# Kernel tuning notes

Measured on AMD Instinct MI355X. Metric: run time of the kernel, lower is better.

## Reference

```python
import jax, jax.numpy as jnp
import numpy as np

EMB = 768
HEADS = 12
HD = EMB // HEADS
FF = 4 * EMB
EPS = 1e-5


def gelu_tanh(x):
    c = jnp.sqrt(jnp.asarray(2.0 / jnp.pi, x.dtype))
    return 0.5 * x * (1.0 + jnp.tanh(c * (x + 0.044715 * x ** 3)))


def layernorm(x, scale, shift):
    mean = x.mean(-1, keepdims=True)
    var = ((x - mean) ** 2).mean(-1, keepdims=True)
    return scale * (x - mean) / jnp.sqrt(var + EPS) + shift


def setup_inputs() -> dict:
    key = jax.random.key(0)
    ks = jax.random.split(key, 12)
    s = 0.02
    return {
        "x": jax.random.normal(ks[0], (8, 1024, EMB), jnp.float32),
        "Wq": jax.random.normal(ks[1], (EMB, EMB), jnp.float32) * s,
        "Wk": jax.random.normal(ks[2], (EMB, EMB), jnp.float32) * s,
        "Wv": jax.random.normal(ks[3], (EMB, EMB), jnp.float32) * s,
        "Wo": jax.random.normal(ks[4], (EMB, EMB), jnp.float32) * s,
        "bo": jnp.zeros((EMB,), jnp.float32),
        "W1": jax.random.normal(ks[5], (EMB, FF), jnp.float32) * s,
        "b1": jnp.zeros((FF,), jnp.float32),
        "W2": jax.random.normal(ks[6], (FF, EMB), jnp.float32) * s,
        "b2": jnp.zeros((EMB,), jnp.float32),
        "ln1_scale": jnp.ones((EMB,), jnp.float32),
        "ln1_shift": jnp.zeros((EMB,), jnp.float32),
        "ln2_scale": jnp.ones((EMB,), jnp.float32),
        "ln2_shift": jnp.zeros((EMB,), jnp.float32),
    }


def reference(x, Wq, Wk, Wv, Wo, bo, W1, b1, W2, b2,
              ln1_scale, ln1_shift, ln2_scale, ln2_shift):
    B, T, _ = x.shape
    inp = x
    h = layernorm(x, ln1_scale, ln1_shift)
    # QKV projections (no bias, qkv_bias=False)
    q = (h @ Wq).reshape(B, T, HEADS, HD).transpose(0, 2, 1, 3)  # [B,H,T,hd]
    k = (h @ Wk).reshape(B, T, HEADS, HD).transpose(0, 2, 1, 3)
    v = (h @ Wv).reshape(B, T, HEADS, HD).transpose(0, 2, 1, 3)
    scores = jnp.einsum('bhqd,bhkd->bhqk', q, k)
    causal = jnp.triu(jnp.ones((T, T), bool), k=1)
    scores = jnp.where(causal, -jnp.inf, scores)
    attn = jax.nn.softmax(scores / jnp.sqrt(jnp.asarray(HD, x.dtype)), axis=-1)
    ctx = jnp.einsum('bhqk,bhkd->bhqd', attn, v)
    ctx = ctx.transpose(0, 2, 1, 3).reshape(B, T, EMB)
    attn_out = ctx @ Wo + bo
    x = inp + attn_out  # dropout is identity (rate 0 / eval)
    inp = x
    h = layernorm(x, ln2_scale, ln2_shift)
    ff = gelu_tanh(h @ W1 + b1) @ W2 + b2
    return inp + ff
```

## Files before the change

kernel.cpp:

```cpp
#include <hip/hip_runtime.h>
#include <hip/hip_bf16.h>
#include <stdint.h>
#include <stddef.h>

#define EMB 768
#define FFD 3072
#define NHEAD 12
#define HD 64
#define SEQ 1024
#define NTOK 8192
#define QKVW 2304

typedef unsigned short u16;
typedef __attribute__((ext_vector_type(8))) short short8;
typedef __attribute__((ext_vector_type(4))) float f32x4;

__device__ __forceinline__ u16 f2bf(float f) {
  union { float f; uint32_t u; } w; w.f = f;
  uint32_t x = w.u + 0x7fffu + ((w.u >> 16) & 1u);
  return (u16)(x >> 16);
}

__device__ __forceinline__ uint32_t pkbf(float lo, float hi) {
  __hip_bfloat162 h = __float22bfloat162_rn(float2{lo, hi});
  union { __hip_bfloat162 h; uint32_t u; } cv; cv.h = h;
  return cv.u;
}

__device__ __forceinline__ void g2l16(const void* g, void* l) {
  __builtin_amdgcn_global_load_lds(
      (const __attribute__((address_space(1))) void*)g,
      (__attribute__((address_space(3))) void*)l, 16, 0, 0);
}

__global__ __launch_bounds__(256)
void transpose_kernel(const float* __restrict__ in, u16* __restrict__ out, int K, int N) {
  __shared__ float tile[32][33];
  const int n0 = blockIdx.x * 32, k0 = blockIdx.y * 32;
  const int tx = threadIdx.x & 31;
  const int ty = threadIdx.x >> 5;
#pragma unroll
  for (int i = 0; i < 32; i += 8)
    tile[ty + i][tx] = in[(size_t)(k0 + ty + i) * N + n0 + tx];
  __syncthreads();
#pragma unroll
  for (int i = 0; i < 32; i += 8)
    out[(size_t)(n0 + ty + i) * K + k0 + tx] = f2bf(tile[tx][ty + i]);
}

__global__ __launch_bounds__(256)
void transpose_qkv_kernel(const float* __restrict__ Wq, const float* __restrict__ Wk,
                          const float* __restrict__ Wv, u16* __restrict__ out) {
  __shared__ float tile[32][33];
  const float* in = blockIdx.z == 0 ? Wq : (blockIdx.z == 1 ? Wk : Wv);
  u16* o = out + (size_t)blockIdx.z * EMB * EMB;
  const int n0 = blockIdx.x * 32, k0 = blockIdx.y * 32;
  const int tx = threadIdx.x & 31;
  const int ty = threadIdx.x >> 5;
#pragma unroll
  for (int i = 0; i < 32; i += 8)
    tile[ty + i][tx] = in[(size_t)(k0 + ty + i) * EMB + n0 + tx];
  __syncthreads();
#pragma unroll
  for (int i = 0; i < 32; i += 8)
    o[(size_t)(n0 + ty + i) * EMB + k0 + tx] = f2bf(tile[tx][ty + i]);
}

__global__ __launch_bounds__(256)
void ln_kernel(const float* __restrict__ x, const float* __restrict__ sc,
               const float* __restrict__ sh, u16* __restrict__ out) {
  const int row = blockIdx.x;
  const int tid = threadIdx.x;
  const float* xr = x + (size_t)row * EMB;
  float v0 = xr[tid], v1 = xr[tid + 256], v2 = xr[tid + 512];
  float s = v0 + v1 + v2;
  float ss = v0 * v0 + v1 * v1 + v2 * v2;
#pragma unroll
  for (int m = 1; m < 64; m <<= 1) { s += __shfl_xor(s, m, 64); ss += __shfl_xor(ss, m, 64); }
  __shared__ float red[8];
  const int wave = tid >> 6, lane = tid & 63;
  if (lane == 0) { red[wave] = s; red[wave + 4] = ss; }
  __syncthreads();
  s = red[0] + red[1] + red[2] + red[3];
  ss = red[4] + red[5] + red[6] + red[7];
  const float mean = s * (1.f / EMB);
  const float var = ss * (1.f / EMB) - mean * mean;
  const float inv = rsqrtf(var + 1e-5f);
  u16* orow = out + (size_t)row * EMB;
  orow[tid]       = f2bf((v0 - mean) * inv * sc[tid]       + sh[tid]);
  orow[tid + 256] = f2bf((v1 - mean) * inv * sc[tid + 256] + sh[tid + 256]);
  orow[tid + 512] = f2bf((v2 - mean) * inv * sc[tid + 512] + sh[tid + 512]);
}

template <int EPI, int MT>
__global__ __launch_bounds__(256)
void gemm_kernel(const u16* __restrict__ A, const u16* __restrict__ BT,
                 void* __restrict__ Cp, const float* __restrict__ bias,
                 const float* __restrict__ res, u16* __restrict__ vTp,
                 int M, int N, int K) {
  constexpr int MI = MT / 32;
  __shared__ u16 As[MT * 64];
  __shared__ u16 Bs[128 * 64];

  const int nwg = gridDim.x * gridDim.y;
  const int orig = blockIdx.y * gridDim.x + blockIdx.x;
  const int swz = (orig & 7) * (nwg >> 3) + (orig >> 3);
  const int m0 = (swz / gridDim.x) * MT;
  const int n0 = (swz % gridDim.x) * 128;

  const int tid = threadIdx.x;
  const int wave = tid >> 6, lane = tid & 63;
  const int wr = wave >> 1, wc = wave & 1;
  const int r = lane & 15, g = lane >> 4;
  const int lrow = lane >> 3;
  const int lelem = (lane & 7) * 8;

  f32x4 acc[MI][4] = {};

  const int nkt = K >> 6;
  for (int kt = 0; kt < nkt; ++kt) {
    const int k0 = kt << 6;
    if (kt) __syncthreads();
#pragma unroll
    for (int q = 0; q < MT / 32; ++q) {
      const int chunk = q * 4 + wave;
      const int row = chunk * 8 + lrow;
      const int e = lelem ^ ((row & 7) << 3);
      g2l16(A + (size_t)(m0 + row) * K + k0 + e, As + chunk * 512);
    }
#pragma unroll
    for (int q = 0; q < 4; ++q) {
      const int chunk = q * 4 + wave;
      const int row = chunk * 8 + lrow;
      const int e = lelem ^ ((row & 7) << 3);
      g2l16(BT + (size_t)(n0 + row) * K + k0 + e, Bs + chunk * 512);
    }
    __syncthreads();
#pragma unroll
    for (int kk = 0; kk < 2; ++kk) {
      short8 af[MI], bf[4];
#pragma unroll
      for (int mi = 0; mi < MI; ++mi) {
        const int row = wr * (MT / 2) + mi * 16 + r;
        af[mi] = *(const short8*)(As + row * 64 + ((kk * 32 + g * 8) ^ ((row & 7) << 3)));
      }
#pragma unroll
      for (int ni = 0; ni < 4; ++ni) {
        const int row = wc * 64 + ni * 16 + r;
        bf[ni] = *(const short8*)(Bs + row * 64 + ((kk * 32 + g * 8) ^ ((row & 7) << 3)));
      }
#pragma unroll
      for (int mi = 0; mi < MI; ++mi)
#pragma unroll
        for (int ni = 0; ni < 4; ++ni)
          acc[mi][ni] = __builtin_amdgcn_mfma_f32_16x16x32_bf16(af[mi], bf[ni], acc[mi][ni], 0, 0, 0);
    }
  }

#pragma unroll
  for (int mi = 0; mi < MI; ++mi)
#pragma unroll
    for (int ni = 0; ni < 4; ++ni) {
      const int rowb = m0 + wr * (MT / 2) + mi * 16 + 4 * g;
      const int col = n0 + wc * 64 + ni * 16 + r;
      if constexpr (EPI == 3) {
        u16 pk[4];
#pragma unroll
        for (int j = 0; j < 4; ++j) pk[j] = f2bf(acc[mi][ni][j]);
        if (col < 1536) {
#pragma unroll
          for (int j = 0; j < 4; ++j)
            ((u16*)Cp)[(size_t)(rowb + j) * N + col] = pk[j];
        } else {
          uint2 w2;
          w2.x = (uint32_t)pk[0] | ((uint32_t)pk[1] << 16);
          w2.y = (uint32_t)pk[2] | ((uint32_t)pk[3] << 16);
          *(uint2*)(vTp + (size_t)(col - 1536) * NTOK + rowb) = w2;
        }
      } else {
#pragma unroll
        for (int j = 0; j < 4; ++j) {
          const size_t idx = (size_t)(rowb + j) * N + col;
          float v = acc[mi][ni][j];
          if constexpr (EPI == 1) {
            ((float*)Cp)[idx] = v + bias[col] + res[idx];
          } else {
            float t = v + bias[col];
            float e = __expf(1.5957691216057308f * (t + 0.044715f * t * t * t));
            float th = 1.f - 2.f / (e + 1.f);
            ((u16*)Cp)[idx] = f2bf(0.5f * t * (1.f + th));
          }
        }
      }
    }
}

#define CEXP 0.18033688011112042f

__global__ __launch_bounds__(256, 3)
void attn_kernel(const u16* __restrict__ qkv, const u16* __restrict__ vT,
                 u16* __restrict__ ctx) {
  const int bh = blockIdx.x;
  const int qt = blockIdx.y;
  const int b = bh / NHEAD, h = bh % NHEAD;
  const int tid = threadIdx.x;
  const int wave = tid >> 6, lane = tid & 63;
  const int r = lane & 15, g = lane >> 4;

  __shared__ u16 Kb[2][64 * 64];
  __shared__ u16 Vb[2][64 * 64];
  __shared__ u16 Pt[4][16 * 64];

  const int qw = qt * 128 + wave * 32;
  const int tok0 = b * SEQ;

  short8 aq[2][2];
#pragma unroll
  for (int qf = 0; qf < 2; ++qf) {
    const u16* qb = qkv + (size_t)(tok0 + qw + qf * 16 + r) * QKVW + h * HD;
    aq[qf][0] = *(const short8*)(qb + g * 8);
    aq[qf][1] = *(const short8*)(qb + 32 + g * 8);
  }

  float l_st[2] = {0.f, 0.f};
  f32x4 oc[2][4] = {};

  const int sr = tid >> 3;
  const int sc = (tid & 7) * 8;
  const int nt = 2 * qt + 2;

  const u16* kg = qkv + (size_t)tok0 * QKVW + EMB + h * HD;
  const u16* vg = vT + (size_t)(h * HD) * NTOK + tok0;
  const int e0 = sc ^ ((sr & 7) << 3);

  auto stage = [&](int buf, int kt) {
    const size_t koff = (size_t)kt * 64;
    u16* kb = (u16*)Kb[buf] + wave * 512;
    u16* vb = (u16*)Vb[buf] + wave * 512;
    g2l16(kg + (koff + sr) * QKVW + e0, kb);
    g2l16(kg + (koff + sr + 32) * QKVW + e0, kb + 2048);
    g2l16(vg + (size_t)sr * NTOK + koff + e0, vb);
    g2l16(vg + (size_t)(sr + 32) * NTOK + koff + e0, vb + 2048);
  };

  stage(0, 0);
  for (int kb = 0; kb < nt; ++kb) {
    __syncthreads();
    const int cur = kb & 1;
    if (kb + 1 < nt) stage(cur ^ 1, kb + 1);

    const int kv0 = kb * 64;
    if (kv0 > qw + 31) continue;

    short8 kf[4][2];
#pragma unroll
    for (int nf = 0; nf < 4; ++nf) {
      const int row = nf * 16 + r;
#pragma unroll
      for (int kk = 0; kk < 2; ++kk)
        kf[nf][kk] = *(const short8*)((char*)Kb[cur] + row * 128 +
                                      ((kk * 64 + g * 16) ^ ((row & 7) << 4)));
    }
    short8 bv[2][4];
#pragma unroll
    for (int half = 0; half < 2; ++half)
#pragma unroll
      for (int nd = 0; nd < 4; ++nd) {
        const int vr = nd * 16 + r;
        bv[half][nd] = *(const short8*)((char*)Vb[cur] + vr * 128 +
                       ((half * 64 + g * 16) ^ ((vr & 7) << 4)));
      }

#pragma unroll
    for (int qf = 0; qf < 2; ++qf) {
      f32x4 st[4];
#pragma unroll
      for (int nf = 0; nf < 4; ++nf) {
        f32x4 z = {};
        z = __builtin_amdgcn_mfma_f32_16x16x32_bf16(kf[nf][0], aq[qf][0], z, 0, 0, 0);
        z = __builtin_amdgcn_mfma_f32_16x16x32_bf16(kf[nf][1], aq[qf][1], z, 0, 0, 0);
        st[nf] = z;
      }
      if (kv0 + 63 > qw + qf * 16) {
        const int qg = qw + qf * 16 + r;
#pragma unroll
        for (int nf = 0; nf < 4; ++nf)
#pragma unroll
          for (int j = 0; j < 4; ++j)
            if (kv0 + nf * 16 + 4 * g + j > qg) st[nf][j] = -3e38f;
      }
      float p[4][4];
      float ps = 0.f;
#pragma unroll
      for (int nf = 0; nf < 4; ++nf)
#pragma unroll
        for (int j = 0; j < 4; ++j) {
          const float pe = exp2f(st[nf][j] * CEXP);
          p[nf][j] = pe;
          ps += pe;
        }
      ps += __shfl_xor(ps, 16);
      ps += __shfl_xor(ps, 32);
      l_st[qf] += ps;

      u16* Pw = (u16*)Pt[wave];
#pragma unroll
      for (int nf = 0; nf < 4; ++nf) {
        uint2 w2;
        w2.x = pkbf(p[nf][0], p[nf][1]);
        w2.y = pkbf(p[nf][2], p[nf][3]);
        *(uint2*)((char*)Pw + r * 128 + ((nf * 32 + g * 8) ^ ((r & 7) << 4))) = w2;
      }
#pragma unroll
      for (int half = 0; half < 2; ++half) {
        short8 pa = *(const short8*)((char*)Pw + r * 128 +
                                     ((half * 64 + g * 16) ^ ((r & 7) << 4)));
#pragma unroll
        for (int nd = 0; nd < 4; ++nd)
          oc[qf][nd] = __builtin_amdgcn_mfma_f32_16x16x32_bf16(pa, bv[half][nd], oc[qf][nd], 0, 0, 0);
      }
    }
  }

#pragma unroll
  for (int qf = 0; qf < 2; ++qf) {
    const float rl = 1.f / l_st[qf];
#pragma unroll
    for (int j = 0; j < 4; ++j) {
      const float rj = __shfl(rl, 4 * g + j, 16);
      const size_t row = (size_t)tok0 + qw + qf * 16 + 4 * g + j;
#pragma unroll
      for (int nd = 0; nd < 4; ++nd)
        ctx[row * EMB + h * HD + nd * 16 + r] = f2bf(oc[qf][nd][j] * rj);
    }
  }
}

extern "C" void kernel_launch(void* const* d_in, const int* in_sizes, int n_in,
                              void* d_out, int out_size, void* d_ws, size_t ws_size,
                              hipStream_t stream) {
  const float* x    = (const float*)d_in[0];
  const float* Wq   = (const float*)d_in[1];
  const float* Wk   = (const float*)d_in[2];
  const float* Wv   = (const float*)d_in[3];
  const float* Wo   = (const float*)d_in[4];
  const float* bo   = (const float*)d_in[5];
  const float* W1   = (const float*)d_in[6];
  const float* b1   = (const float*)d_in[7];
  const float* W2   = (const float*)d_in[8];
  const float* b2   = (const float*)d_in[9];
  const float* ln1s = (const float*)d_in[10];
  const float* ln1b = (const float*)d_in[11];
  const float* ln2s = (const float*)d_in[12];
  const float* ln2b = (const float*)d_in[13];

  char* p = (char*)d_ws;
  u16* qkvT = (u16*)p; p += (size_t)QKVW * EMB * 2;
  u16* woT  = (u16*)p; p += (size_t)EMB * EMB * 2;
  u16* w1T  = (u16*)p; p += (size_t)FFD * EMB * 2;
  u16* w2T  = (u16*)p; p += (size_t)EMB * FFD * 2;
  u16* h1   = (u16*)p; p += (size_t)NTOK * EMB * 2;
  u16* qkv  = (u16*)p; p += (size_t)NTOK * QKVW * 2;
  float* x2 = (float*)p; p += (size_t)NTOK * EMB * 4;
  u16* ff1  = (u16*)p; p += (size_t)NTOK * FFD * 2;
  u16* ctxb = h1;
  u16* h2   = qkv;
  u16* vT   = ff1;

  if (ws_size < (size_t)(p - (char*)d_ws)) return;

  dim3 blk(256);
  transpose_qkv_kernel<<<dim3(24, 24, 3), blk, 0, stream>>>(Wq, Wk, Wv, qkvT);
  transpose_kernel<<<dim3(24, 24), blk, 0, stream>>>(Wo, woT, EMB, EMB);
  transpose_kernel<<<dim3(96, 24), blk, 0, stream>>>(W1, w1T, EMB, FFD);
  transpose_kernel<<<dim3(24, 96), blk, 0, stream>>>(W2, w2T, FFD, EMB);

  ln_kernel<<<NTOK, blk, 0, stream>>>(x, ln1s, ln1b, h1);
  gemm_kernel<3, 128><<<dim3(18, 64), blk, 0, stream>>>(h1, qkvT, qkv, nullptr, nullptr, vT, NTOK, QKVW, EMB);
  attn_kernel<<<dim3(96, 8), blk, 0, stream>>>(qkv, vT, ctxb);
  gemm_kernel<1, 64><<<dim3(6, 128), blk, 0, stream>>>(ctxb, woT, x2, bo, x, nullptr, NTOK, EMB, EMB);
  ln_kernel<<<NTOK, blk, 0, stream>>>(x2, ln2s, ln2b, h2);
  gemm_kernel<2, 128><<<dim3(24, 64), blk, 0, stream>>>(h2, w1T, ff1, b1, nullptr, nullptr, NTOK, FFD, EMB);
  gemm_kernel<1, 64><<<dim3(6, 128), blk, 0, stream>>>(ff1, w2T, (float*)d_out, b2, x2, nullptr, NTOK, EMB, FFD);
}
```

Measured before the change: 239.9 us.

## Add 256x256 double-buffered 8-wave GEMM for QKV and FF1 projections

Adds a new GEMM kernel with 256x256 output tiles and 512 threads. It double-buffers LDS in 64-wide K tiles, issuing the next tile's global-to-LDS loads in four quarter-stages interleaved with MFMA work, using explicit vmcnt waits and raised scheduling priority. The QKV and FF1 projections now use it, aiming for more data reuse per tile and load/compute overlap. In exchange the kernel uses 128KB of LDS and many accumulator registers, and the QKV grid shrinks to 288 workgroups, which may leave some of the chip idle.

```diff
diff --git a/kernel.cpp b/kernel.cpp
--- a/kernel.cpp
+++ b/kernel.cpp
@@ -32,6 +32,9 @@
       (const __attribute__((address_space(1))) void*)g,
       (__attribute__((address_space(3))) void*)l, 16, 0, 0);
 }
+
+#define VMCNT(n) asm volatile("s_waitcnt vmcnt(" #n ")" ::: "memory")
+#define LGKM0()  asm volatile("s_waitcnt lgkmcnt(0)" ::: "memory")
 
 __global__ __launch_bounds__(256)
 void transpose_kernel(const float* __restrict__ in, u16* __restrict__ out, int K, int N) {
@@ -92,77 +95,136 @@
   orow[tid + 512] = f2bf((v2 - mean) * inv * sc[tid + 512] + sh[tid + 512]);
 }
 
-template <int EPI, int MT>
-__global__ __launch_bounds__(256)
-void gemm_kernel(const u16* __restrict__ A, const u16* __restrict__ BT,
-                 void* __restrict__ Cp, const float* __restrict__ bias,
-                 const float* __restrict__ res, u16* __restrict__ vTp,
-                 int M, int N, int K) {
-  constexpr int MI = MT / 32;
-  __shared__ u16 As[MT * 64];
-  __shared__ u16 Bs[128 * 64];
+template <int EPI>
+__global__ __launch_bounds__(512, 2)
+void gemm256_kernel(const u16* __restrict__ A, const u16* __restrict__ BT,
+                    void* __restrict__ Cp, const float* __restrict__ bias,
+                    u16* __restrict__ vTp, int M, int N, int K) {
+  __shared__ u16 sm[65536];
 
   const int nwg = gridDim.x * gridDim.y;
   const int orig = blockIdx.y * gridDim.x + blockIdx.x;
-  const int swz = (orig & 7) * (nwg >> 3) + (orig >> 3);
-  const int m0 = (swz / gridDim.x) * MT;
-  const int n0 = (swz % gridDim.x) * 128;
+  const int swzb = (orig & 7) * (nwg >> 3) + (orig >> 3);
+  const int m0 = (swzb / gridDim.x) * 256;
+  const int n0 = (swzb % gridDim.x) * 256;
 
   const int tid = threadIdx.x;
-  const int wave = tid >> 6, lane = tid & 63;
-  const int wr = wave >> 1, wc = wave & 1;
+  const int w = tid >> 6, lane = tid & 63;
+  const int wm = w >> 2, wn = w & 3;
   const int r = lane & 15, g = lane >> 4;
-  const int lrow = lane >> 3;
-  const int lelem = (lane & 7) * 8;
-
-  f32x4 acc[MI][4] = {};
-
-  const int nkt = K >> 6;
-  for (int kt = 0; kt < nkt; ++kt) {
-    const int k0 = kt << 6;
-    if (kt) __syncthreads();
-#pragma unroll
-    for (int q = 0; q < MT / 32; ++q) {
-      const int chunk = q * 4 + wave;
-      const int row = chunk * 8 + lrow;
-      const int e = lelem ^ ((row & 7) << 3);
-      g2l16(A + (size_t)(m0 + row) * K + k0 + e, As + chunk * 512);
-    }
-#pragma unroll
-    for (int q = 0; q < 4; ++q) {
-      const int chunk = q * 4 + wave;
-      const int row = chunk * 8 + lrow;
-      const int e = lelem ^ ((row & 7) << 3);
-      g2l16(BT + (size_t)(n0 + row) * K + k0 + e, Bs + chunk * 512);
-    }
-    __syncthreads();
-#pragma unroll
-    for (int kk = 0; kk < 2; ++kk) {
-      short8 af[MI], bf[4];
-#pragma unroll
-      for (int mi = 0; mi < MI; ++mi) {
-        const int row = wr * (MT / 2) + mi * 16 + r;
-        af[mi] = *(const short8*)(As + row * 64 + ((kk * 32 + g * 8) ^ ((row & 7) << 3)));
-      }
-#pragma unroll
-      for (int ni = 0; ni < 4; ++ni) {
-        const int row = wc * 64 + ni * 16 + r;
-        bf[ni] = *(const short8*)(Bs + row * 64 + ((kk * 32 + g * 8) ^ ((row & 7) << 3)));
-      }
-#pragma unroll
-      for (int mi = 0; mi < MI; ++mi)
-#pragma unroll
-        for (int ni = 0; ni < 4; ++ni)
-          acc[mi][ni] = __builtin_amdgcn_mfma_f32_16x16x32_bf16(af[mi], bf[ni], acc[mi][ni], 0, 0, 0);
+  const int sr = tid >> 3;
+  const int scw = ((tid & 7) * 8) ^ ((sr & 7) << 3);
+
+  f32x4 acc[8][4] = {};
+
+  const int NT = K >> 6;
+
+  auto stageA = [&](int p, int h, int t) {
+    u16* dst = sm + (p * 2 + h) * 8192 + (w * 8) * 64;
+    const u16* src = A + (size_t)(m0 + h * 64 + sr) * K + t * 64 + scw;
+    g2l16(src, dst);
+    g2l16(src + (size_t)128 * K, dst + 4096);
+  };
+  auto stageB = [&](int p, int h, int t) {
+    u16* dst = sm + 32768 + (p * 2 + h) * 8192 + (w * 8) * 64;
+    const int gr0 = h * 32 + (sr >> 5) * 64 + (sr & 31);
+    const u16* src = BT + (size_t)(n0 + gr0) * K + t * 64 + scw;
+    g2l16(src, dst);
+    g2l16(src + (size_t)128 * K, dst + 4096);
+  };
+
+  auto lda = [&](int p, int mh, short8 af[2][4]) {
+    const u16* base = sm + (p * 2 + mh) * 8192;
+#pragma unroll
+    for (int kk = 0; kk < 2; ++kk)
+#pragma unroll
+      for (int mi2 = 0; mi2 < 4; ++mi2) {
+        const int lr = wm * 64 + mi2 * 16 + r;
+        af[kk][mi2] = *(const short8*)(base + lr * 64 + ((kk * 32 + g * 8) ^ ((r & 7) << 3)));
+      }
+  };
+  auto ldb = [&](int p, int nh, short8 bf[2][2]) {
+    const u16* base = sm + 32768 + (p * 2 + nh) * 8192;
+#pragma unroll
+    for (int kk = 0; kk < 2; ++kk)
+#pragma unroll
+      for (int nf2 = 0; nf2 < 2; ++nf2) {
+        const int lr = wn * 32 + nf2 * 16 + r;
+        bf[kk][nf2] = *(const short8*)(base + lr * 64 + ((kk * 32 + g * 8) ^ ((r & 7) << 3)));
+      }
+  };
+  auto mfma16 = [&](int mh, int nh, short8 af[2][4], short8 bf[2][2]) {
+    __builtin_amdgcn_s_setprio(1);
+#pragma unroll
+    for (int kk = 0; kk < 2; ++kk)
+#pragma unroll
+      for (int mi2 = 0; mi2 < 4; ++mi2)
+#pragma unroll
+        for (int nf2 = 0; nf2 < 2; ++nf2)
+          acc[mh * 4 + mi2][nh * 2 + nf2] = __builtin_amdgcn_mfma_f32_16x16x32_bf16(
+              af[kk][mi2], bf[kk][nf2], acc[mh * 4 + mi2][nh * 2 + nf2], 0, 0, 0);
+    __builtin_amdgcn_s_setprio(0);
+  };
+
+  stageA(0, 0, 0); stageB(0, 0, 0); stageB(0, 1, 0); stageA(0, 1, 0);
+  VMCNT(4);
+  __builtin_amdgcn_s_barrier();
+
+  for (int t = 0; t < NT - 1; ++t) {
+    const int p = t & 1;
+    {
+      short8 af[2][4], bf[2][2];
+      lda(p, 0, af); ldb(p, 0, bf);
+      stageA(p ^ 1, 0, t + 1);
+      VMCNT(4); __builtin_amdgcn_s_barrier();
+      mfma16(0, 0, af, bf);
+      LGKM0(); __builtin_amdgcn_s_barrier();
+    }
+    {
+      short8 af[2][4], bf[2][2];
+      lda(p, 0, af); ldb(p, 1, bf);
+      stageB(p ^ 1, 0, t + 1);
+      VMCNT(4); __builtin_amdgcn_s_barrier();
+      mfma16(0, 1, af, bf);
+      LGKM0(); __builtin_amdgcn_s_barrier();
+    }
+    {
+      short8 af[2][4], bf[2][2];
+      lda(p, 1, af); ldb(p, 0, bf);
+      stageB(p ^ 1, 1, t + 1);
+      VMCNT(4); __builtin_amdgcn_s_barrier();
+      mfma16(1, 0, af, bf);
+      LGKM0(); __builtin_amdgcn_s_barrier();
+    }
+    {
+      short8 af[2][4], bf[2][2];
+      lda(p, 1, af); ldb(p, 1, bf);
+      stageA(p ^ 1, 1, t + 1);
+      VMCNT(4); __builtin_amdgcn_s_barrier();
+      mfma16(1, 1, af, bf);
+      LGKM0(); __builtin_amdgcn_s_barrier();
     }
   }
-
-#pragma unroll
-  for (int mi = 0; mi < MI; ++mi)
+  {
+    const int p = (NT - 1) & 1;
+    VMCNT(0);
+    __builtin_amdgcn_s_barrier();
+#pragma unroll
+    for (int mh = 0; mh < 2; ++mh)
+#pragma unroll
+      for (int nh = 0; nh < 2; ++nh) {
+        short8 af[2][4], bf[2][2];
+        lda(p, mh, af); ldb(p, nh, bf);
+        mfma16(mh, nh, af, bf);
+      }
+  }
+
+#pragma unroll
+  for (int mi = 0; mi < 8; ++mi)
 #pragma unroll
     for (int ni = 0; ni < 4; ++ni) {
-      const int rowb = m0 + wr * (MT / 2) + mi * 16 + 4 * g;
-      const int col = n0 + wc * 64 + ni * 16 + r;
+      const int rowb = m0 + wm * 128 + mi * 16 + 4 * g;
+      const int col = n0 + wn * 64 + ni * 16 + r;
       if constexpr (EPI == 3) {
         u16 pk[4];
 #pragma unroll
@@ -180,19 +242,90 @@
       } else {
 #pragma unroll
         for (int j = 0; j < 4; ++j) {
-          const size_t idx = (size_t)(rowb + j) * N + col;
-          float v = acc[mi][ni][j];
-          if constexpr (EPI == 1) {
-            ((float*)Cp)[idx] = v + bias[col] + res[idx];
-          } else {
-            float t = v + bias[col];
-            float e = __expf(1.5957691216057308f * (t + 0.044715f * t * t * t));
-            float th = 1.f - 2.f / (e + 1.f);
-            ((u16*)Cp)[idx] = f2bf(0.5f * t * (1.f + th));
-          }
+          float t = acc[mi][ni][j] + bias[col];
+          float e = __expf(1.5957691216057308f * (t + 0.044715f * t * t * t));
+          float th = 1.f - 2.f / (e + 1.f);
+          ((u16*)Cp)[(size_t)(rowb + j) * N + col] = f2bf(0.5f * t * (1.f + th));
         }
       }
     }
+}
+
+template <int EPI, int MT>
+__global__ __launch_bounds__(256)
+void gemm_kernel(const u16* __restrict__ A, const u16* __restrict__ BT,
+                 void* __restrict__ Cp, const float* __restrict__ bias,
+                 const float* __restrict__ res, int M, int N, int K) {
+  constexpr int MI = MT / 32;
+  __shared__ u16 As[MT * 64];
+  __shared__ u16 Bs[128 * 64];
+
+  const int nwg = gridDim.x * gridDim.y;
+  const int orig = blockIdx.y * gridDim.x + blockIdx.x;
+  const int swz = (orig & 7) * (nwg >> 3) + (orig >> 3);
+  const int m0 = (swz / gridDim.x) * MT;
+  const int n0 = (swz % gridDim.x) * 128;
+
+  const int tid = threadIdx.x;
+  const int wave = tid >> 6, lane = tid & 63;
+  const int wr = wave >> 1, wc = wave & 1;
+  const int r = lane & 15, g = lane >> 4;
+  const int lrow = lane >> 3;
+  const int lelem = (lane & 7) * 8;
+
+  f32x4 acc[MI][4] = {};
+
+  const int nkt = K >> 6;
+  for (int kt = 0; kt < nkt; ++kt) {
+    const int k0 = kt << 6;
+    if (kt) __syncthreads();
+#pragma unroll
+    for (int q = 0; q < MT / 32; ++q) {
+      const int chunk = q * 4 + wave;
+      const int row = chunk * 8 + lrow;
+      const int e = lelem ^ ((row & 7) << 3);
+      g2l16(A + (size_t)(m0 + row) * K + k0 + e, As + chunk * 512);
+    }
+#pragma unroll
+    for (int q = 0; q < 4; ++q) {
+      const int chunk = q * 4 + wave;
+      const int row = chunk * 8 + lrow;
+      const int e = lelem ^ ((row & 7) << 3);
+      g2l16(BT + (size_t)(n0 + row) * K + k0 + e, Bs + chunk * 512);
+    }
+    __syncthreads();
+#pragma unroll
+    for (int kk = 0; kk < 2; ++kk) {
+      short8 af[MI], bf[4];
+#pragma unroll
+      for (int mi = 0; mi < MI; ++mi) {
+        const int row = wr * (MT / 2) + mi * 16 + r;
+        af[mi] = *(const short8*)(As + row * 64 + ((kk * 32 + g * 8) ^ ((row & 7) << 3)));
+      }
+#pragma unroll
+      for (int ni = 0; ni < 4; ++ni) {
+        const int row = wc * 64 + ni * 16 + r;
+        bf[ni] = *(const short8*)(Bs + row * 64 + ((kk * 32 + g * 8) ^ ((row & 7) << 3)));
+      }
+#pragma unroll
+      for (int mi = 0; mi < MI; ++mi)
+#pragma unroll
+        for (int ni = 0; ni < 4; ++ni)
+          acc[mi][ni] = __builtin_amdgcn_mfma_f32_16x16x32_bf16(af[mi], bf[ni], acc[mi][ni], 0, 0, 0);
+    }
+  }
+
+#pragma unroll
+  for (int mi = 0; mi < MI; ++mi)
+#pragma unroll
+    for (int ni = 0; ni < 4; ++ni)
+#pragma unroll
+      for (int j = 0; j < 4; ++j) {
+        const int row = m0 + wr * (MT / 2) + mi * 16 + 4 * g + j;
+        const int col = n0 + wc * 64 + ni * 16 + r;
+        const size_t idx = (size_t)row * N + col;
+        ((float*)Cp)[idx] = acc[mi][ni][j] + bias[col] + res[idx];
+      }
 }
 
 #define CEXP 0.18033688011112042f
@@ -376,10 +509,10 @@
   transpose_kernel<<<dim3(24, 96), blk, 0, stream>>>(W2, w2T, FFD, EMB);
 
   ln_kernel<<<NTOK, blk, 0, stream>>>(x, ln1s, ln1b, h1);
-  gemm_kernel<3, 128><<<dim3(18, 64), blk, 0, stream>>>(h1, qkvT, qkv, nullptr, nullptr, vT, NTOK, QKVW, EMB);
+  gemm256_kernel<3><<<dim3(9, 32), dim3(512), 0, stream>>>(h1, qkvT, qkv, nullptr, vT, NTOK, QKVW, EMB);
   attn_kernel<<<dim3(96, 8), blk, 0, stream>>>(qkv, vT, ctxb);
-  gemm_kernel<1, 64><<<dim3(6, 128), blk, 0, stream>>>(ctxb, woT, x2, bo, x, nullptr, NTOK, EMB, EMB);
+  gemm_kernel<1, 64><<<dim3(6, 128), blk, 0, stream>>>(ctxb, woT, x2, bo, x, NTOK, EMB, EMB);
   ln_kernel<<<NTOK, blk, 0, stream>>>(x2, ln2s, ln2b, h2);
-  gemm_kernel<2, 128><<<dim3(24, 64), blk, 0, stream>>>(h2, w1T, ff1, b1, nullptr, nullptr, NTOK, FFD, EMB);
-  gemm_kernel<1, 64><<<dim3(6, 128), blk, 0, stream>>>(ff1, w2T, (float*)d_out, b2, x2, nullptr, NTOK, EMB, FFD);
-}
+  gemm256_kernel<2><<<dim3(12, 32), dim3(512), 0, stream>>>(h2, w1T, ff1, b1, nullptr, NTOK, FFD, EMB);
+  gemm_kernel<1, 64><<<dim3(6, 128), blk, 0, stream>>>(ff1, w2T, (float*)d_out, b2, x2, NTOK, EMB, FFD);
+}
```

Result: slower. 277.8 us (+15.8%).

## Switch GEMM to 32x32x16 MFMA tiles with compile-time shapes

Applied to the files above, without the earlier changes.

Moves the GEMM inner loop from 16x16x32 to 32x32x16 bf16 MFMA instructions and reworks the fragment loads and the epilogue index mapping to match the 32x32 output layout. Problem dimensions become template parameters, so the tile swizzle and loop trip counts are constants at compile time. The larger MFMA shape is meant to reduce LDS fragment reads per FLOP and per-instruction issue overhead. In exchange, each lane now writes output elements scattered across rows in the epilogue, and the bigger accumulator raises register pressure.

```diff
diff --git a/kernel.cpp b/kernel.cpp
--- a/kernel.cpp
+++ b/kernel.cpp
@@ -14,6 +14,7 @@
 typedef unsigned short u16;
 typedef __attribute__((ext_vector_type(8))) short short8;
 typedef __attribute__((ext_vector_type(4))) float f32x4;
+typedef __attribute__((ext_vector_type(16))) float f32x16;
 
 __device__ __forceinline__ u16 f2bf(float f) {
   union { float f; uint32_t u; } w; w.f = f;
@@ -92,34 +93,34 @@
   orow[tid + 512] = f2bf((v2 - mean) * inv * sc[tid + 512] + sh[tid + 512]);
 }
 
-template <int EPI, int MT>
+template <int EPI, int MT, int M, int N, int K>
 __global__ __launch_bounds__(256)
 void gemm_kernel(const u16* __restrict__ A, const u16* __restrict__ BT,
                  void* __restrict__ Cp, const float* __restrict__ bias,
-                 const float* __restrict__ res, u16* __restrict__ vTp,
-                 int M, int N, int K) {
-  constexpr int MI = MT / 32;
+                 const float* __restrict__ res, u16* __restrict__ vTp) {
+  constexpr int MI = MT / 64;
   __shared__ u16 As[MT * 64];
   __shared__ u16 Bs[128 * 64];
 
-  const int nwg = gridDim.x * gridDim.y;
-  const int orig = blockIdx.y * gridDim.x + blockIdx.x;
-  const int swz = (orig & 7) * (nwg >> 3) + (orig >> 3);
-  const int m0 = (swz / gridDim.x) * MT;
-  const int n0 = (swz % gridDim.x) * 128;
+  constexpr int GX = N / 128;
+  constexpr int NWG = GX * (M / MT);
+  const int orig = blockIdx.y * GX + blockIdx.x;
+  const int swz = (orig & 7) * (NWG >> 3) + (orig >> 3);
+  const int m0 = (swz / GX) * MT;
+  const int n0 = (swz % GX) * 128;
 
   const int tid = threadIdx.x;
   const int wave = tid >> 6, lane = tid & 63;
   const int wr = wave >> 1, wc = wave & 1;
-  const int r = lane & 15, g = lane >> 4;
+  const int c32 = lane & 31, hi = lane >> 5;
   const int lrow = lane >> 3;
   const int lelem = (lane & 7) * 8;
 
-  f32x4 acc[MI][4] = {};
-
-  const int nkt = K >> 6;
-  for (int kt = 0; kt < nkt; ++kt) {
-    const int k0 = kt << 6;
+  f32x16 acc[MI][2] = {};
+
+  constexpr int NKT = K / 64;
+  for (int kt = 0; kt < NKT; ++kt) {
+    const int k0 = kt * 64;
     if (kt) __syncthreads();
 #pragma unroll
     for (int q = 0; q < MT / 32; ++q) {
@@ -137,59 +138,74 @@
     }
     __syncthreads();
 #pragma unroll
-    for (int kk = 0; kk < 2; ++kk) {
-      short8 af[MI], bf[4];
+    for (int ks = 0; ks < 4; ++ks) {
+      short8 af[MI], bf[2];
 #pragma unroll
       for (int mi = 0; mi < MI; ++mi) {
-        const int row = wr * (MT / 2) + mi * 16 + r;
-        af[mi] = *(const short8*)(As + row * 64 + ((kk * 32 + g * 8) ^ ((row & 7) << 3)));
-      }
-#pragma unroll
-      for (int ni = 0; ni < 4; ++ni) {
-        const int row = wc * 64 + ni * 16 + r;
-        bf[ni] = *(const short8*)(Bs + row * 64 + ((kk * 32 + g * 8) ^ ((row & 7) << 3)));
+        const int row = wr * (MT / 2) + mi * 32 + c32;
+        af[mi] = *(const short8*)(As + row * 64 + ((ks * 16 + hi * 8) ^ ((row & 7) << 3)));
+      }
+#pragma unroll
+      for (int ni = 0; ni < 2; ++ni) {
+        const int row = wc * 64 + ni * 32 + c32;
+        bf[ni] = *(const short8*)(Bs + row * 64 + ((ks * 16 + hi * 8) ^ ((row & 7) << 3)));
       }
 #pragma unroll
       for (int mi = 0; mi < MI; ++mi)
 #pragma unroll
-        for (int ni = 0; ni < 4; ++ni)
-          acc[mi][ni] = __builtin_amdgcn_mfma_f32_16x16x32_bf16(af[mi], bf[ni], acc[mi][ni], 0, 0, 0);
+        for (int ni = 0; ni < 2; ++ni)
+          acc[mi][ni] = __builtin_amdgcn_mfma_f32_32x32x16_bf16(af[mi], bf[ni], acc[mi][ni], 0, 0, 0);
     }
   }
 
 #pragma unroll
   for (int mi = 0; mi < MI; ++mi)
 #pragma unroll
-    for (int ni = 0; ni < 4; ++ni) {
-      const int rowb = m0 + wr * (MT / 2) + mi * 16 + 4 * g;
-      const int col = n0 + wc * 64 + ni * 16 + r;
+    for (int ni = 0; ni < 2; ++ni) {
+      const int rb = m0 + wr * (MT / 2) + mi * 32 + 4 * hi;
+      const int col = n0 + wc * 64 + ni * 32 + c32;
       if constexpr (EPI == 3) {
-        u16 pk[4];
-#pragma unroll
-        for (int j = 0; j < 4; ++j) pk[j] = f2bf(acc[mi][ni][j]);
         if (col < 1536) {
 #pragma unroll
-          for (int j = 0; j < 4; ++j)
-            ((u16*)Cp)[(size_t)(rowb + j) * N + col] = pk[j];
+          for (int q = 0; q < 16; q += 2) {
+            const int r0 = rb + (q & 3) + 8 * (q >> 2);
+            const uint32_t pk = pkbf(acc[mi][ni][q], acc[mi][ni][q + 1]);
+            ((u16*)Cp)[(size_t)r0 * N + col] = (u16)pk;
+            ((u16*)Cp)[(size_t)(r0 + 1) * N + col] = (u16)(pk >> 16);
+          }
         } else {
-          uint2 w2;
-          w2.x = (uint32_t)pk[0] | ((uint32_t)pk[1] << 16);
-          w2.y = (uint32_t)pk[2] | ((uint32_t)pk[3] << 16);
-          *(uint2*)(vTp + (size_t)(col - 1536) * NTOK + rowb) = w2;
+#pragma unroll
+          for (int qd = 0; qd < 4; ++qd) {
+            const int r0 = rb + 8 * qd;
+            uint2 w2;
+            w2.x = pkbf(acc[mi][ni][qd * 4 + 0], acc[mi][ni][qd * 4 + 1]);
+            w2.y = pkbf(acc[mi][ni][qd * 4 + 2], acc[mi][ni][qd * 4 + 3]);
+            *(uint2*)(vTp + (size_t)(col - 1536) * NTOK + r0) = w2;
+          }
+        }
+      } else if constexpr (EPI == 1) {
+        const float bc = bias[col];
+#pragma unroll
+        for (int q = 0; q < 16; ++q) {
+          const int rr = rb + (q & 3) + 8 * (q >> 2);
+          const size_t idx = (size_t)rr * N + col;
+          ((float*)Cp)[idx] = acc[mi][ni][q] + bc + res[idx];
         }
       } else {
-#pragma unroll
-        for (int j = 0; j < 4; ++j) {
-          const size_t idx = (size_t)(rowb + j) * N + col;
-          float v = acc[mi][ni][j];
-          if constexpr (EPI == 1) {
-            ((float*)Cp)[idx] = v + bias[col] + res[idx];
-          } else {
-            float t = v + bias[col];
+        const float bc = bias[col];
+#pragma unroll
+        for (int q = 0; q < 16; q += 2) {
+          const int r0 = rb + (q & 3) + 8 * (q >> 2);
+          float tj[2];
+#pragma unroll
+          for (int j = 0; j < 2; ++j) {
+            float t = acc[mi][ni][q + j] + bc;
             float e = __expf(1.5957691216057308f * (t + 0.044715f * t * t * t));
-            float th = 1.f - 2.f / (e + 1.f);
-            ((u16*)Cp)[idx] = f2bf(0.5f * t * (1.f + th));
+            tj[j] = 0.5f * t * (1.f + (1.f - 2.f / (e + 1.f)));
           }
+          const uint32_t pk = pkbf(tj[0], tj[1]);
+          ((u16*)Cp)[(size_t)r0 * N + col] = (u16)pk;
+          ((u16*)Cp)[(size_t)(r0 + 1) * N + col] = (u16)(pk >> 16);
         }
       }
     }
@@ -376,10 +392,10 @@
   transpose_kernel<<<dim3(24, 96), blk, 0, stream>>>(W2, w2T, FFD, EMB);
 
   ln_kernel<<<NTOK, blk, 0, stream>>>(x, ln1s, ln1b, h1);
-  gemm_kernel<3, 128><<<dim3(18, 64), blk, 0, stream>>>(h1, qkvT, qkv, nullptr, nullptr, vT, NTOK, QKVW, EMB);
+  gemm_kernel<3, 128, NTOK, QKVW, EMB><<<dim3(18, 64), blk, 0, stream>>>(h1, qkvT, qkv, nullptr, nullptr, vT);
   attn_kernel<<<dim3(96, 8), blk, 0, stream>>>(qkv, vT, ctxb);
-  gemm_kernel<1, 64><<<dim3(6, 128), blk, 0, stream>>>(ctxb, woT, x2, bo, x, nullptr, NTOK, EMB, EMB);
+  gemm_kernel<1, 64, NTOK, EMB, EMB><<<dim3(6, 128), blk, 0, stream>>>(ctxb, woT, x2, bo, x, nullptr);
   ln_kernel<<<NTOK, blk, 0, stream>>>(x2, ln2s, ln2b, h2);
-  gemm_kernel<2, 128><<<dim3(24, 64), blk, 0, stream>>>(h2, w1T, ff1, b1, nullptr, nullptr, NTOK, FFD, EMB);
-  gemm_kernel<1, 64><<<dim3(6, 128), blk, 0, stream>>>(ff1, w2T, (float*)d_out, b2, x2, nullptr, NTOK, EMB, FFD);
-}
+  gemm_kernel<2, 128, NTOK, FFD, EMB><<<dim3(24, 64), blk, 0, stream>>>(h2, w1T, ff1, b1, nullptr, nullptr);
+  gemm_kernel<1, 64, NTOK, EMB, FFD><<<dim3(6, 128), blk, 0, stream>>>(ff1, w2T, (float*)d_out, b2, x2, nullptr);
+}
```

Measured after the change: 249.3 us. +3.9%, slower.
